# Kernel optimization log

Hardware: AMD Instinct MI355X
Metric: run time of the kernel (lower is better)

Reference implementation:

```python
import jax, jax.numpy as jnp
import numpy as np
import math

D_MODEL = 1024
N_HEADS = 16
HEAD_DIM = D_MODEL // N_HEADS
SEQ_LEN = 8192
INCLUDE_LOCAL = 2


def get_dilated_positions(seq_len, include_local=2):
    # Faithful numpy port of the torch pattern generator (runs once at setup).
    max_attend = include_local + int(math.ceil(math.log2(seq_len + 1)))
    positions = np.zeros((seq_len, max_attend), dtype=np.int64)
    mask = np.zeros((seq_len, max_attend), dtype=bool)
    for i in range(seq_len):
        ap = [i]
        for j in range(1, include_local + 1):
            if i - j >= 0:
                ap.append(i - j)
        k = 2
        while i - 2 ** k >= 0:
            ap.append(i - 2 ** k)
            k += 1
        positions[i, :len(ap)] = ap
        mask[i, :len(ap)] = True
    return positions, mask


def setup_inputs() -> dict:
    key = jax.random.key(0)
    kx, kq, kk, kv, ko = jax.random.split(key, 5)
    x = jax.random.normal(kx, (1, SEQ_LEN, D_MODEL), dtype=jnp.float32)
    # nn.Linear(bias=False) weights, torch layout [out_features, in_features]
    s = 0.02
    q_w = jax.random.normal(kq, (D_MODEL, D_MODEL), dtype=jnp.float32) * s
    k_w = jax.random.normal(kk, (D_MODEL, D_MODEL), dtype=jnp.float32) * s
    v_w = jax.random.normal(kv, (D_MODEL, D_MODEL), dtype=jnp.float32) * s
    o_w = jax.random.normal(ko, (D_MODEL, D_MODEL), dtype=jnp.float32) * s
    pos_np, mask_np = get_dilated_positions(SEQ_LEN, INCLUDE_LOCAL)
    return {
        "x": x,
        "q_w": q_w, "k_w": k_w, "v_w": v_w, "o_w": o_w,
        "positions": jnp.asarray(pos_np),   # (S, A) int64 indices
        "attend_mask": jnp.asarray(mask_np) # (S, A) bool
    }


def reference(x, q_w, k_w, v_w, o_w, positions, attend_mask):
    B, S, _ = x.shape
    H, Dh = N_HEADS, HEAD_DIM
    scale = Dh ** -0.5

    q = (x @ q_w.T).reshape(B, S, H, Dh).transpose(0, 2, 1, 3)  # (B,H,S,Dh)
    k = (x @ k_w.T).reshape(B, S, H, Dh).transpose(0, 2, 1, 3)
    v = (x @ v_w.T).reshape(B, S, H, Dh).transpose(0, 2, 1, 3)

    # Gather K/V at the dilated positions: (B,H,S,A,Dh)
    k_sparse = k[:, :, positions, :]
    v_sparse = v[:, :, positions, :]

    scores = jnp.einsum('bhsd,bhsad->bhsa', q, k_sparse) * scale
    scores = jnp.where(attend_mask[None, None, :, :], scores, -jnp.inf)
    attn = jax.nn.softmax(scores, axis=-1)  # dropout p in eval / 0.0 -> identity

    out = jnp.einsum('bhsa,bhsad->bhsd', attn, v_sparse)
    out = out.transpose(0, 2, 1, 3).reshape(B, S, D_MODEL)
    return out @ o_w.T
```

## Files before the change

kernel.cpp:

```cpp
#include <hip/hip_runtime.h>
#include <hip/hip_bf16.h>

typedef __bf16 bf16_t;
typedef __bf16 bf16x4 __attribute__((ext_vector_type(4)));
typedef __bf16 bf16x8 __attribute__((ext_vector_type(8)));
typedef float floatx16 __attribute__((ext_vector_type(16)));

#define SEQ    8192
#define DM     1024
#define NHEADS 16
#define HDIM   64

__device__ __forceinline__ void async_ld16(bf16_t* lds, const bf16_t* g) {
  __builtin_amdgcn_global_load_lds(
      (__attribute__((address_space(1))) void*)g,
      (__attribute__((address_space(3))) void*)lds, 16, 0, 0);
}

__global__ __launch_bounds__(256)
void cvt_all(const float* __restrict__ x,  const float* __restrict__ qw,
             const float* __restrict__ kw, const float* __restrict__ vw,
             const float* __restrict__ ow,
             bf16_t* __restrict__ Xb,  bf16_t* __restrict__ QWb,
             bf16_t* __restrict__ KWb, bf16_t* __restrict__ VWb,
             bf16_t* __restrict__ OWb) {
  const int b = blockIdx.x;
  const float* in; bf16_t* out; int g;
  if (b < 8192) { in = x; out = Xb; g = b; }
  else {
    const int w  = (b - 8192) >> 10;
    const int wb = (b - 8192) & 1023;
    switch (w) {
      case 0:  in = qw; out = QWb; break;
      case 1:  in = kw; out = KWb; break;
      case 2:  in = vw; out = VWb; break;
      default: in = ow; out = OWb; break;
    }
    g = wb;
  }
  const int idx = (g * 256 + threadIdx.x) * 4;
  float4 v = *(const float4*)(in + idx);
  bf16x4 o = { (bf16_t)v.x, (bf16_t)v.y, (bf16_t)v.z, (bf16_t)v.w };
  *(bf16x4*)(out + idx) = o;
}

__global__ __launch_bounds__(256)
void gemm_qkv(const bf16_t* __restrict__ A,
              const bf16_t* __restrict__ Bq, const bf16_t* __restrict__ Bk,
              const bf16_t* __restrict__ Bv,
              bf16_t* __restrict__ Cq, bf16_t* __restrict__ Ck, bf16_t* __restrict__ Cv)
{
  const bf16_t* B = (blockIdx.z == 0) ? Bq : (blockIdx.z == 1) ? Bk : Bv;
  bf16_t*       C = (blockIdx.z == 0) ? Cq : (blockIdx.z == 1) ? Ck : Cv;
  constexpr int Kdim = DM;
  __shared__ __attribute__((aligned(16))) bf16_t sA[128 * 64];
  __shared__ __attribute__((aligned(16))) bf16_t sB[128 * 64];

  const int tid  = threadIdx.x;
  const int wave = tid >> 6;
  const int lane = tid & 63;
  const int l31  = lane & 31;
  const int half = lane >> 5;
  const int wr   = (wave >> 1) * 64;
  const int wc   = (wave & 1) * 64;

  const int gc = (lane & 7) ^ ((lane >> 3) & 7);
  const size_t arow0 = (size_t)blockIdx.x * 128 + wave * 32 + (lane >> 3);
  const size_t brow0 = (size_t)blockIdx.y * 128 + wave * 32 + (lane >> 3);
  const bf16_t* Ag = A + arow0 * Kdim + gc * 8;
  const bf16_t* Bg = B + brow0 * Kdim + gc * 8;
  bf16_t* sAw = sA + wave * 32 * 64;
  bf16_t* sBw = sB + wave * 32 * 64;

  floatx16 acc[2][2];
  #pragma unroll
  for (int i = 0; i < 2; ++i)
    #pragma unroll
    for (int j = 0; j < 2; ++j)
      acc[i][j] = (floatx16)(0.0f);

  const int sw = l31 & 7;

  for (int ko = 0; ko < Kdim; ko += 64) {
    #pragma unroll
    for (int n = 0; n < 4; ++n) {
      async_ld16(sAw + n * 512, Ag + (size_t)n * 8 * Kdim + ko);
      async_ld16(sBw + n * 512, Bg + (size_t)n * 8 * Kdim + ko);
    }
    __syncthreads();

    #pragma unroll
    for (int s = 0; s < 4; ++s) {
      const int ck   = s * 2 + half;
      const int slot = (ck ^ sw) * 8;
      bf16x8 af[2], bfr[2];
      #pragma unroll
      for (int mi = 0; mi < 2; ++mi)
        af[mi] = *(const bf16x8*)&sA[(wr + mi * 32 + l31) * 64 + slot];
      #pragma unroll
      for (int ni = 0; ni < 2; ++ni)
        bfr[ni] = *(const bf16x8*)&sB[(wc + ni * 32 + l31) * 64 + slot];

      #pragma unroll
      for (int mi = 0; mi < 2; ++mi)
        #pragma unroll
        for (int ni = 0; ni < 2; ++ni)
          acc[mi][ni] = __builtin_amdgcn_mfma_f32_32x32x16_bf16(af[mi], bfr[ni], acc[mi][ni], 0, 0, 0);
    }

    __syncthreads();
  }

  const float scl = (blockIdx.z == 0) ? 0.125f : 1.0f;
  const int crow0 = blockIdx.x * 128 + wr + 4 * half;
  const int ccol0 = blockIdx.y * 128 + wc + l31;
  #pragma unroll
  for (int mi = 0; mi < 2; ++mi)
    #pragma unroll
    for (int ni = 0; ni < 2; ++ni)
      #pragma unroll
      for (int r = 0; r < 16; ++r) {
        const int row = crow0 + mi * 32 + (r & 3) + 8 * (r >> 2);
        C[(size_t)row * DM + (ccol0 + ni * 32)] = (bf16_t)(acc[mi][ni][r] * scl);
      }
}

__global__ __launch_bounds__(256)
void gemm_out(const bf16_t* __restrict__ A, const bf16_t* __restrict__ B,
              float* __restrict__ C)
{
  constexpr int Kdim = DM;
  __shared__ __attribute__((aligned(16))) bf16_t sA[128 * 32];
  __shared__ __attribute__((aligned(16))) bf16_t sB[64 * 32];

  const int tid  = threadIdx.x;
  const int wave = tid >> 6;
  const int lane = tid & 63;
  const int l31  = lane & 31;
  const int half = lane >> 5;
  const int wr   = (wave >> 1) * 64;
  const int wc   = (wave & 1) * 32;

  const int gc = (lane & 3) ^ ((lane >> 3) & 3);
  const size_t arow = (size_t)blockIdx.x * 128 + wave * 32 + (lane >> 2);
  const size_t brow = (size_t)blockIdx.y * 64 + wave * 16 + (lane >> 2);
  const bf16_t* Ag = A + arow * Kdim + gc * 8;
  const bf16_t* Bg = B + brow * Kdim + gc * 8;
  bf16_t* sAw = sA + wave * 32 * 32;
  bf16_t* sBw = sB + wave * 16 * 32;

  floatx16 acc[2];
  acc[0] = (floatx16)(0.0f);
  acc[1] = (floatx16)(0.0f);

  const int sw = (l31 >> 1) & 3;

  for (int ko = 0; ko < Kdim; ko += 32) {
    async_ld16(sAw,           Ag + ko);
    async_ld16(sAw + 16 * 32, Ag + 16 * Kdim + ko);
    async_ld16(sBw,           Bg + ko);
    __syncthreads();

    #pragma unroll
    for (int s = 0; s < 2; ++s) {
      const int ck   = s * 2 + half;
      const int slot = (ck ^ sw) * 8;
      bf16x8 af[2], bfr;
      #pragma unroll
      for (int mi = 0; mi < 2; ++mi)
        af[mi] = *(const bf16x8*)&sA[(wr + mi * 32 + l31) * 32 + slot];
      bfr = *(const bf16x8*)&sB[(wc + l31) * 32 + slot];

      #pragma unroll
      for (int mi = 0; mi < 2; ++mi)
        acc[mi] = __builtin_amdgcn_mfma_f32_32x32x16_bf16(af[mi], bfr, acc[mi], 0, 0, 0);
    }

    __syncthreads();
  }

  const int crow0 = blockIdx.x * 128 + wr + 4 * half;
  const int ccol  = blockIdx.y * 64 + wc + l31;
  #pragma unroll
  for (int mi = 0; mi < 2; ++mi)
    #pragma unroll
    for (int r = 0; r < 16; ++r) {
      const int row = crow0 + mi * 32 + (r & 3) + 8 * (r >> 2);
      C[(size_t)row * DM + ccol] = acc[mi][r];
    }
}

__global__ __launch_bounds__(256)
void dilated_attn(const bf16_t* __restrict__ Q, const bf16_t* __restrict__ K,
                  const bf16_t* __restrict__ V, bf16_t* O)
{
  __shared__ float sM[2][64];
  __shared__ float sL[2][64];
  __shared__ float sAcc[2][64][17];

  const int lane = threadIdx.x & 63;
  const int wv   = threadIdx.x >> 6;
  const int ql   = wv >> 1;
  const int sub  = wv & 1;
  const int qb   = (blockIdx.x & 7) * 512 + (blockIdx.x >> 3);
  const int i    = qb * 2 + ql;
  const size_t base = (size_t)i * DM + lane * 16;

  bf16x8 q0 = *(const bf16x8*)(Q + base);
  bf16x8 q1 = *(const bf16x8*)(Q + base + 8);
  float qf[16];
  #pragma unroll
  for (int j = 0; j < 8; ++j) { qf[j] = (float)q0[j]; qf[j + 8] = (float)q1[j]; }

  const int npos = (i == 0) ? 1 : (33 - __builtin_clz((unsigned)i));
  auto pos_addr = [&](int t) -> size_t {
    const int off = (t == 0) ? 0 : (1 << (t - 1));
    return (size_t)(i - off) * DM + lane * 16;
  };

  float m = -INFINITY, l = 0.0f;
  float acc[16];
  #pragma unroll
  for (int j = 0; j < 16; ++j) acc[j] = 0.0f;

  int t = sub;
  if (t < npos) {
    size_t a = pos_addr(t);
    bf16x8 k0 = *(const bf16x8*)(K + a), k1 = *(const bf16x8*)(K + a + 8);
    bf16x8 v0 = *(const bf16x8*)(V + a), v1 = *(const bf16x8*)(V + a + 8);
    while (true) {
      const int tn = t + 2;
      const bool more = (tn < npos);
      bf16x8 nk0, nk1, nv0, nv1;
      if (more) {
        const size_t na = pos_addr(tn);
        nk0 = *(const bf16x8*)(K + na); nk1 = *(const bf16x8*)(K + na + 8);
        nv0 = *(const bf16x8*)(V + na); nv1 = *(const bf16x8*)(V + na + 8);
      }

      float sc = 0.0f;
      #pragma unroll
      for (int j = 0; j < 8; ++j) sc += qf[j] * (float)k0[j] + qf[j + 8] * (float)k1[j];
      sc += __shfl_xor(sc, 1, 64);
      sc += __shfl_xor(sc, 2, 64);

      float mn = fmaxf(m, sc);
      float co = __expf(m - mn);
      float w  = __expf(sc - mn);
      l = l * co + w;
      m = mn;
      #pragma unroll
      for (int j = 0; j < 8; ++j) {
        acc[j]     = acc[j]     * co + w * (float)v0[j];
        acc[j + 8] = acc[j + 8] * co + w * (float)v1[j];
      }

      if (!more) break;
      k0 = nk0; k1 = nk1; v0 = nv0; v1 = nv1;
      t = tn;
    }
  }

  if (sub == 1) {
    sM[ql][lane] = m;
    sL[ql][lane] = l;
    #pragma unroll
    for (int j = 0; j < 16; ++j) sAcc[ql][lane][j] = acc[j];
  }
  __syncthreads();
  if (sub == 0) {
    const float mb = sM[ql][lane], lb = sL[ql][lane];
    const float mt = fmaxf(m, mb);
    const float ca = __expf(m - mt);
    const float cb = __expf(mb - mt);
    const float inv = 1.0f / (l * ca + lb * cb);
    bf16x8 o0, o1;
    #pragma unroll
    for (int j = 0; j < 8; ++j) {
      o0[j] = (bf16_t)((acc[j]     * ca + sAcc[ql][lane][j]     * cb) * inv);
      o1[j] = (bf16_t)((acc[j + 8] * ca + sAcc[ql][lane][j + 8] * cb) * inv);
    }
    *(bf16x8*)(O + base)     = o0;
    *(bf16x8*)(O + base + 8) = o1;
  }
}

extern "C" void kernel_launch(void* const* d_in, const int* in_sizes, int n_in,
                              void* d_out, int out_size, void* d_ws, size_t ws_size,
                              hipStream_t stream) {
  (void)in_sizes; (void)n_in; (void)out_size; (void)ws_size;
  const float* x  = (const float*)d_in[0];
  const float* qw = (const float*)d_in[1];
  const float* kw = (const float*)d_in[2];
  const float* vw = (const float*)d_in[3];
  const float* ow = (const float*)d_in[4];
  float* out = (float*)d_out;

  bf16_t* Xb  = (bf16_t*)d_ws;
  bf16_t* Qb  = Xb  + (size_t)SEQ * DM;
  bf16_t* Kb  = Qb  + (size_t)SEQ * DM;
  bf16_t* Vb  = Kb  + (size_t)SEQ * DM;
  bf16_t* QWb = Vb  + (size_t)SEQ * DM;
  bf16_t* KWb = QWb + (size_t)DM * DM;
  bf16_t* VWb = KWb + (size_t)DM * DM;
  bf16_t* OWb = VWb + (size_t)DM * DM;
  bf16_t* AO  = Qb;

  cvt_all<<<dim3(8192 + 4096), dim3(256), 0, stream>>>(x, qw, kw, vw, ow,
                                                       Xb, QWb, KWb, VWb, OWb);

  dim3 block(256);
  gemm_qkv<<<dim3(SEQ / 128, DM / 128, 3), block, 0, stream>>>(Xb, QWb, KWb, VWb, Qb, Kb, Vb);
  dilated_attn<<<dim3(SEQ / 2), block, 0, stream>>>(Qb, Kb, Vb, AO);
  gemm_out<<<dim3(SEQ / 128, DM / 64), block, 0, stream>>>(AO, OWb, out);
}
```

Baseline: 215.9 us.

## Split QKV GEMM into three launches, widen attention splits, reuse 128 tile for output

The fused z-indexed QKV GEMM becomes three separate launches of a shared templated 128x128 core. The output projection now uses that same 128x128 tile in place of its earlier 128x64 tile with K-step 32. The attention kernel grows to 512 threads, with four waves per query that each handle every fourth dilated position, then merges the partial softmax states through LDS. The aim is more parallelism per query and fewer distinct kernels, at the cost of extra launches, halving the output GEMM grid, and more LDS per attention block.

```diff
diff --git a/kernel.cpp b/kernel.cpp
--- a/kernel.cpp
+++ b/kernel.cpp
@@ -44,14 +44,11 @@
   *(bf16x4*)(out + idx) = o;
 }
 
-__global__ __launch_bounds__(256)
-void gemm_qkv(const bf16_t* __restrict__ A,
-              const bf16_t* __restrict__ Bq, const bf16_t* __restrict__ Bk,
-              const bf16_t* __restrict__ Bv,
-              bf16_t* __restrict__ Cq, bf16_t* __restrict__ Ck, bf16_t* __restrict__ Cv)
-{
-  const bf16_t* B = (blockIdx.z == 0) ? Bq : (blockIdx.z == 1) ? Bk : Bv;
-  bf16_t*       C = (blockIdx.z == 0) ? Cq : (blockIdx.z == 1) ? Ck : Cv;
+template <typename OutT>
+__device__ __forceinline__ void gemm128_core(
+    const bf16_t* __restrict__ A, const bf16_t* __restrict__ B,
+    OutT* __restrict__ C, float scl)
+{
   constexpr int Kdim = DM;
   __shared__ __attribute__((aligned(16))) bf16_t sA[128 * 64];
   __shared__ __attribute__((aligned(16))) bf16_t sB[128 * 64];
@@ -111,7 +108,6 @@
     __syncthreads();
   }
 
-  const float scl = (blockIdx.z == 0) ? 0.125f : 1.0f;
   const int crow0 = blockIdx.x * 128 + wr + 4 * half;
   const int ccol0 = blockIdx.y * 128 + wc + l31;
   #pragma unroll
@@ -121,87 +117,36 @@
       #pragma unroll
       for (int r = 0; r < 16; ++r) {
         const int row = crow0 + mi * 32 + (r & 3) + 8 * (r >> 2);
-        C[(size_t)row * DM + (ccol0 + ni * 32)] = (bf16_t)(acc[mi][ni][r] * scl);
+        C[(size_t)row * DM + (ccol0 + ni * 32)] = (OutT)(acc[mi][ni][r] * scl);
       }
 }
 
 __global__ __launch_bounds__(256)
-void gemm_out(const bf16_t* __restrict__ A, const bf16_t* __restrict__ B,
-              float* __restrict__ C)
-{
-  constexpr int Kdim = DM;
-  __shared__ __attribute__((aligned(16))) bf16_t sA[128 * 32];
-  __shared__ __attribute__((aligned(16))) bf16_t sB[64 * 32];
-
-  const int tid  = threadIdx.x;
-  const int wave = tid >> 6;
-  const int lane = tid & 63;
-  const int l31  = lane & 31;
-  const int half = lane >> 5;
-  const int wr   = (wave >> 1) * 64;
-  const int wc   = (wave & 1) * 32;
-
-  const int gc = (lane & 3) ^ ((lane >> 3) & 3);
-  const size_t arow = (size_t)blockIdx.x * 128 + wave * 32 + (lane >> 2);
-  const size_t brow = (size_t)blockIdx.y * 64 + wave * 16 + (lane >> 2);
-  const bf16_t* Ag = A + arow * Kdim + gc * 8;
-  const bf16_t* Bg = B + brow * Kdim + gc * 8;
-  bf16_t* sAw = sA + wave * 32 * 32;
-  bf16_t* sBw = sB + wave * 16 * 32;
-
-  floatx16 acc[2];
-  acc[0] = (floatx16)(0.0f);
-  acc[1] = (floatx16)(0.0f);
-
-  const int sw = (l31 >> 1) & 3;
-
-  for (int ko = 0; ko < Kdim; ko += 32) {
-    async_ld16(sAw,           Ag + ko);
-    async_ld16(sAw + 16 * 32, Ag + 16 * Kdim + ko);
-    async_ld16(sBw,           Bg + ko);
-    __syncthreads();
-
-    #pragma unroll
-    for (int s = 0; s < 2; ++s) {
-      const int ck   = s * 2 + half;
-      const int slot = (ck ^ sw) * 8;
-      bf16x8 af[2], bfr;
-      #pragma unroll
-      for (int mi = 0; mi < 2; ++mi)
-        af[mi] = *(const bf16x8*)&sA[(wr + mi * 32 + l31) * 32 + slot];
-      bfr = *(const bf16x8*)&sB[(wc + l31) * 32 + slot];
-
-      #pragma unroll
-      for (int mi = 0; mi < 2; ++mi)
-        acc[mi] = __builtin_amdgcn_mfma_f32_32x32x16_bf16(af[mi], bfr, acc[mi], 0, 0, 0);
-    }
-
-    __syncthreads();
-  }
-
-  const int crow0 = blockIdx.x * 128 + wr + 4 * half;
-  const int ccol  = blockIdx.y * 64 + wc + l31;
-  #pragma unroll
-  for (int mi = 0; mi < 2; ++mi)
-    #pragma unroll
-    for (int r = 0; r < 16; ++r) {
-      const int row = crow0 + mi * 32 + (r & 3) + 8 * (r >> 2);
-      C[(size_t)row * DM + ccol] = acc[mi][r];
-    }
+void gemm_proj(const bf16_t* __restrict__ A, const bf16_t* __restrict__ B,
+               bf16_t* __restrict__ C, float scl)
+{
+  gemm128_core<bf16_t>(A, B, C, scl);
 }
 
 __global__ __launch_bounds__(256)
+void gemm_outk(const bf16_t* __restrict__ A, const bf16_t* __restrict__ B,
+               float* __restrict__ C)
+{
+  gemm128_core<float>(A, B, C, 1.0f);
+}
+
+__global__ __launch_bounds__(512)
 void dilated_attn(const bf16_t* __restrict__ Q, const bf16_t* __restrict__ K,
                   const bf16_t* __restrict__ V, bf16_t* O)
 {
-  __shared__ float sM[2][64];
-  __shared__ float sL[2][64];
-  __shared__ float sAcc[2][64][17];
+  __shared__ float sM[3][2][64];
+  __shared__ float sL[3][2][64];
+  __shared__ float sAcc[3][2][64][17];
 
   const int lane = threadIdx.x & 63;
   const int wv   = threadIdx.x >> 6;
-  const int ql   = wv >> 1;
-  const int sub  = wv & 1;
+  const int ql   = wv >> 2;
+  const int sub  = wv & 3;
   const int qb   = (blockIdx.x & 7) * 512 + (blockIdx.x >> 3);
   const int i    = qb * 2 + ql;
   const size_t base = (size_t)i * DM + lane * 16;
@@ -229,7 +174,7 @@
     bf16x8 k0 = *(const bf16x8*)(K + a), k1 = *(const bf16x8*)(K + a + 8);
     bf16x8 v0 = *(const bf16x8*)(V + a), v1 = *(const bf16x8*)(V + a + 8);
     while (true) {
-      const int tn = t + 2;
+      const int tn = t + 4;
       const bool more = (tn < npos);
       bf16x8 nk0, nk1, nv0, nv1;
       if (more) {
@@ -261,24 +206,32 @@
     }
   }
 
-  if (sub == 1) {
-    sM[ql][lane] = m;
-    sL[ql][lane] = l;
-    #pragma unroll
-    for (int j = 0; j < 16; ++j) sAcc[ql][lane][j] = acc[j];
+  if (sub != 0) {
+    sM[sub - 1][ql][lane] = m;
+    sL[sub - 1][ql][lane] = l;
+    #pragma unroll
+    for (int j = 0; j < 16; ++j) sAcc[sub - 1][ql][lane][j] = acc[j];
   }
   __syncthreads();
   if (sub == 0) {
-    const float mb = sM[ql][lane], lb = sL[ql][lane];
-    const float mt = fmaxf(m, mb);
-    const float ca = __expf(m - mt);
-    const float cb = __expf(mb - mt);
-    const float inv = 1.0f / (l * ca + lb * cb);
+    #pragma unroll
+    for (int p = 0; p < 3; ++p) {
+      const float mb = sM[p][ql][lane], lb = sL[p][ql][lane];
+      const float mt = fmaxf(m, mb);
+      const float ca = __expf(m - mt);
+      const float cb = __expf(mb - mt);
+      l = l * ca + lb * cb;
+      #pragma unroll
+      for (int j = 0; j < 16; ++j)
+        acc[j] = acc[j] * ca + sAcc[p][ql][lane][j] * cb;
+      m = mt;
+    }
+    const float inv = 1.0f / l;
     bf16x8 o0, o1;
     #pragma unroll
     for (int j = 0; j < 8; ++j) {
-      o0[j] = (bf16_t)((acc[j]     * ca + sAcc[ql][lane][j]     * cb) * inv);
-      o1[j] = (bf16_t)((acc[j + 8] * ca + sAcc[ql][lane][j + 8] * cb) * inv);
+      o0[j] = (bf16_t)(acc[j]     * inv);
+      o1[j] = (bf16_t)(acc[j + 8] * inv);
     }
     *(bf16x8*)(O + base)     = o0;
     *(bf16x8*)(O + base + 8) = o1;
@@ -309,8 +262,10 @@
   cvt_all<<<dim3(8192 + 4096), dim3(256), 0, stream>>>(x, qw, kw, vw, ow,
                                                        Xb, QWb, KWb, VWb, OWb);
 
-  dim3 block(256);
-  gemm_qkv<<<dim3(SEQ / 128, DM / 128, 3), block, 0, stream>>>(Xb, QWb, KWb, VWb, Qb, Kb, Vb);
-  dilated_attn<<<dim3(SEQ / 2), block, 0, stream>>>(Qb, Kb, Vb, AO);
-  gemm_out<<<dim3(SEQ / 128, DM / 64), block, 0, stream>>>(AO, OWb, out);
-}
+  dim3 pg(SEQ / 128, DM / 128);
+  gemm_proj<<<pg, dim3(256), 0, stream>>>(Xb, QWb, Qb, 0.125f);
+  gemm_proj<<<pg, dim3(256), 0, stream>>>(Xb, KWb, Kb, 1.0f);
+  gemm_proj<<<pg, dim3(256), 0, stream>>>(Xb, VWb, Vb, 1.0f);
+  dilated_attn<<<dim3(SEQ / 2), dim3(512), 0, stream>>>(Qb, Kb, Vb, AO);
+  gemm_outk<<<pg, dim3(256), 0, stream>>>(AO, OWb, out);
+}
```

Measured after the change: 226.4 us. 4.8% more time.
